# Performance work log

Hardware: AMD Instinct MI355X
Metric: run time of the kernel (lower is better)

## Reference

```python
import jax, jax.numpy as jnp
import numpy as np

GROUP_SIZE = 64  # quantization group size along in_features
RANK = 16
ALPHA = 1.0


def setup_inputs() -> dict:
    key = jax.random.key(0)
    ks = jax.random.split(key, 7)
    B, S, D_in, D_out = 4, 2048, 4096, 4096
    n_groups = D_in // GROUP_SIZE
    x = jax.random.normal(ks[0], (B, S, D_in), dtype=jnp.float32)
    qweight = jax.random.randint(ks[1], (D_out, D_in), 0, 16, dtype=jnp.int32)
    scales = jax.random.uniform(ks[2], (D_out, n_groups), dtype=jnp.float32) * 0.02
    zeros = jax.random.uniform(ks[3], (D_out, n_groups), dtype=jnp.float32) * 16.0
    lora_A = jax.random.normal(ks[4], (RANK, D_in), dtype=jnp.float32) / np.sqrt(D_in)
    lora_B = jax.random.normal(ks[5], (D_out, RANK), dtype=jnp.float32) * 0.01
    bias = jax.random.normal(ks[6], (D_out,), dtype=jnp.float32) * 0.02
    return {"x": x, "qweight": qweight, "scales": scales, "zeros": zeros,
            "lora_A": lora_A, "lora_B": lora_B, "bias": bias}


def _dequant(qweight, scales, zeros):
    # qweight: [O, I] int codes in [0,16); scales/zeros: [O, G] with G = I // GROUP_SIZE
    O, I = qweight.shape
    G = I // GROUP_SIZE
    q = qweight.astype(scales.dtype).reshape(O, G, GROUP_SIZE)
    w = (q - zeros[:, :, None]) * scales[:, :, None]
    return w.reshape(O, I)


def reference(x, qweight, scales, zeros, lora_A, lora_B, bias):
    # Base 4-bit dequantized matmul: y = x @ W^T
    W = _dequant(qweight, scales, zeros)            # [O, I]
    y = jnp.einsum('bsi,oi->bso', x, W)             # [B, S, O]
    # LoRA low-rank update: (alpha / rank) * (x @ A^T) @ B^T
    scaling = ALPHA / RANK
    lora = jnp.einsum('bsr,or->bso', jnp.einsum('bsi,ri->bsr', x, lora_A), lora_B)
    return y + scaling * lora + bias
```

## Files before the change

### kernel.cpp

```cpp
#include <hip/hip_runtime.h>
#include <stdint.h>
#include <stddef.h>

#define GM 8192
#define GN 4096
#define GK 4096
#define NGRP 64

typedef __bf16 bf16;
typedef __attribute__((ext_vector_type(8))) __bf16 bf16x8;
typedef __attribute__((ext_vector_type(4))) __bf16 bf16x4;
typedef __attribute__((ext_vector_type(4))) float floatx4;
typedef __attribute__((ext_vector_type(4))) int   intx4;
typedef __attribute__((ext_vector_type(8))) unsigned short ushortx8;
typedef __attribute__((ext_vector_type(4))) unsigned short ushortx4;

__device__ inline unsigned short f2bf(float f) {
  unsigned int u = __builtin_bit_cast(unsigned int, f);
  u += 0x7FFFu + ((u >> 16) & 1u);
  return (unsigned short)(u >> 16);
}
__device__ inline bf16x8 pack8(floatx4 a, floatx4 b) {
  ushortx8 u;
  u[0]=f2bf(a[0]); u[1]=f2bf(a[1]); u[2]=f2bf(a[2]); u[3]=f2bf(a[3]);
  u[4]=f2bf(b[0]); u[5]=f2bf(b[1]); u[6]=f2bf(b[2]); u[7]=f2bf(b[3]);
  return __builtin_bit_cast(bf16x8, u);
}
__device__ inline bf16x4 pack4(floatx4 a) {
  ushortx4 u;
  u[0]=f2bf(a[0]); u[1]=f2bf(a[1]); u[2]=f2bf(a[2]); u[3]=f2bf(a[3]);
  return __builtin_bit_cast(bf16x4, u);
}
__device__ inline void gll16(const void* g, void* l) {
  __builtin_amdgcn_global_load_lds(
      (const __attribute__((address_space(1))) void*)g,
      (__attribute__((address_space(3))) void*)l, 16, 0, 0);
}


__global__ __launch_bounds__(256) void qlora_prep_w(
    const int* __restrict__ qw, const float* __restrict__ scales,
    const float* __restrict__ zeros, const float* __restrict__ lA,
    const float* __restrict__ lB, bf16* __restrict__ wbf) {
  __shared__ __align__(16) float Al[16 * 256];
  __shared__ __align__(16) float Bl[32 * 16];
  const int tid = threadIdx.x;
  const int n0  = (blockIdx.x & 127) * 32;
  const int kc0 = (blockIdx.x >> 7) * 256;
  #pragma unroll
  for (int t = 0; t < 4; ++t) {
    int idx = tid + t * 256;
    int r = idx >> 6, c = idx & 63;
    *(floatx4*)&Al[r * 256 + c * 4] = *(const floatx4*)&lA[(size_t)r * GK + kc0 + c * 4];
  }
  if (tid < 128) {
    int r = tid >> 2, c = tid & 3;
    *(floatx4*)&Bl[r * 16 + c * 4] = *(const floatx4*)&lB[(size_t)(n0 + r) * 16 + c * 4];
  }
  __syncthreads();

  const int klane = tid & 63;
  const int wv    = tid >> 6;
  const int k  = klane * 4;
  const int kg = kc0 + k;
  const int kb = kg & ~63;
  const int g  = kg >> 6;

  floatx4 lacc[8] = {};
  #pragma unroll
  for (int r = 0; r < 16; ++r) {
    floatx4 av = *(const floatx4*)&Al[r * 256 + k];
    #pragma unroll
    for (int it = 0; it < 8; ++it)
      lacc[it] += av * Bl[(wv * 8 + it) * 16 + r];
  }

  #pragma unroll
  for (int it = 0; it < 8; ++it) {
    int n  = n0 + wv * 8 + it;
    intx4 qv = *(const intx4*)&qw[(size_t)n * GK + kg];
    float s = scales[n * NGRP + g];
    float z = zeros[n * NGRP + g];
    floatx4 w;
    w[0] = ((float)qv[0] - z) * s + 0.0625f * lacc[it][0];
    w[1] = ((float)qv[1] - z) * s + 0.0625f * lacc[it][1];
    w[2] = ((float)qv[2] - z) * s + 0.0625f * lacc[it][2];
    w[3] = ((float)qv[3] - z) * s + 0.0625f * lacc[it][3];
    int p = (((kg >> 3) & 7) ^ (n & 7)) << 3;
    *(bf16x4*)&wbf[(size_t)n * GK + kb + p + (kg & 7)] = pack4(w);
  }
}

__global__ __launch_bounds__(256) void qlora_prep_x(
    const float* __restrict__ x, bf16* __restrict__ xbf) {
  const int tid = threadIdx.x;
  const int xb  = blockIdx.x;
  #pragma unroll
  for (int t = 0; t < 4; ++t) {
    int fc = xb * 1024 + t * 256 + tid;
    int m  = fc >> 9;
    int rc = fc & 511;
    int p  = (rc & 7) ^ (m & 7);
    const float* src = x + ((size_t)fc << 3);
    floatx4 a = *(const floatx4*)src;
    floatx4 b = *(const floatx4*)(src + 4);
    *(bf16x8*)(xbf + (size_t)m * GK + ((rc >> 3) << 6) + (p << 3)) = pack8(a, b);
  }
}

__global__ __launch_bounds__(512, 1) void qlora_gemm_pre(
    const bf16* __restrict__ Abf, const bf16* __restrict__ Wbf,
    const float* __restrict__ bias, float* __restrict__ out) {
  __shared__ __align__(16) bf16 As[2][256 * 64];
  __shared__ __align__(16) bf16 Bs[2][256 * 64];
  const int tid  = threadIdx.x;
  const int wave = tid >> 6;
  const int lane = tid & 63;
  const int wr   = wave >> 2;
  const int wc   = wave & 3;

  const int flat = blockIdx.x;
  const int xcd  = flat & 7;
  const int j    = flat >> 3;
  const int m0   = (j >> 1) * 256;
  const int n0   = (xcd * 2 + (j & 1)) * 256;

  const int srow = tid >> 3;
  const int schk = tid & 7;
  const bf16* gA = Abf + (size_t)(m0 + srow) * GK + schk * 8;
  const bf16* gB = Wbf + (size_t)(n0 + srow) * GK + schk * 8;
  char* lA = (char*)&As[0][0] + srow * 128 + schk * 16;
  char* lB = (char*)&Bs[0][0] + srow * 128 + schk * 16;

  auto stageA = [&](int buf, int tk, int half) {
    #pragma unroll
    for (int r = 0; r < 2; ++r) {
      int rb = half * 128 + r * 64;
      gll16(gA + (size_t)rb * GK + tk * 64, lA + buf * 32768 + rb * 128);
    }
  };
  auto stageB = [&](int buf, int tk, int half) {
    #pragma unroll
    for (int r = 0; r < 2; ++r) {
      int rb = half * 128 + r * 64;
      gll16(gB + (size_t)rb * GK + tk * 64, lB + buf * 32768 + rb * 128);
    }
  };

  const int rs   = lane & 7;
  const int hi   = lane >> 4;
  const int rofs = (lane & 15) * 64;
  const int c0   = ((0 + hi) ^ rs) << 3;
  const int c1   = ((4 + hi) ^ rs) << 3;
  const int arow = wr * 64;
  const int brow = wc * 32;

  bf16x8 a0[4][2], a1[4][2], b0[2][2], b1[2][2];
  floatx4 acc[8][4] = {};

#define RD_A(DST, P, MH) { \
    const bf16* Ap_ = &As[P][(MH * 128 + arow) * 64 + rofs]; \
    _Pragma("unroll") \
    for (int mi = 0; mi < 4; ++mi) { \
      DST[mi][0] = *(const bf16x8*)(Ap_ + mi * 16 * 64 + c0); \
      DST[mi][1] = *(const bf16x8*)(Ap_ + mi * 16 * 64 + c1); \
    } }
#define RD_B(DST, P, NH) { \
    const bf16* Bp_ = &Bs[P][(NH * 128 + brow) * 64 + rofs]; \
    _Pragma("unroll") \
    for (int ni = 0; ni < 2; ++ni) { \
      DST[ni][0] = *(const bf16x8*)(Bp_ + ni * 16 * 64 + c0); \
      DST[ni][1] = *(const bf16x8*)(Bp_ + ni * 16 * 64 + c1); \
    } }
#define MFMA_PH(MH, NH, AR, BR) { \
    _Pragma("unroll") \
    for (int kk = 0; kk < 2; ++kk) \
      _Pragma("unroll") \
      for (int mi = 0; mi < 4; ++mi) \
        _Pragma("unroll") \
        for (int ni = 0; ni < 2; ++ni) \
          acc[MH * 4 + mi][NH * 2 + ni] = __builtin_amdgcn_mfma_f32_16x16x32_bf16( \
              AR[mi][kk], BR[ni][kk], acc[MH * 4 + mi][NH * 2 + ni], 0, 0, 0); \
  }
#define BAR() __builtin_amdgcn_s_barrier()
#define LGKM0() asm volatile("s_waitcnt lgkmcnt(0)" ::: "memory")
#define PRIO(N) __builtin_amdgcn_s_setprio(N)

  stageA(0, 0, 0); stageA(0, 0, 1); stageB(0, 0, 0); stageB(0, 0, 1);
  stageA(1, 1, 0); stageB(1, 1, 1); stageA(1, 1, 1);
  asm volatile("s_waitcnt vmcnt(6)" ::: "memory");
  BAR();

  for (int t = 0; t < 64; ++t) {
    const int p = t & 1;
    RD_A(a0, p, 0); RD_B(b0, p, 0);
    if (t < 63) stageB(1 - p, t + 1, 0);
    BAR(); LGKM0();
    PRIO(1); MFMA_PH(0, 0, a0, b0); PRIO(0);
    RD_B(b1, p, 1);
    BAR();
    if (t < 62) stageA(p, t + 2, 0);
    BAR(); LGKM0();
    PRIO(1); MFMA_PH(0, 1, a0, b1); PRIO(0);
    RD_A(a1, p, 1);
    BAR();
    if (t < 62) stageB(p, t + 2, 1);
    BAR(); LGKM0();
    PRIO(1); MFMA_PH(1, 1, a1, b1); PRIO(0);
    BAR();
    if (t < 62) {
      stageA(p, t + 2, 1);
      asm volatile("s_waitcnt vmcnt(6)" ::: "memory");
    } else {
      asm volatile("s_waitcnt vmcnt(0)" ::: "memory");
    }
    BAR();
    PRIO(1); MFMA_PH(1, 0, a1, b0); PRIO(0);
    BAR();
  }

#undef RD_A
#undef RD_B
#undef MFMA_PH
#undef BAR
#undef LGKM0
#undef PRIO

  const int quad = lane >> 4;
  const int col  = lane & 15;
  #pragma unroll
  for (int nh = 0; nh < 2; ++nh)
    #pragma unroll
    for (int ni = 0; ni < 2; ++ni) {
      const int gn = n0 + nh * 128 + wc * 32 + ni * 16 + col;
      const float bvv = bias[gn];
      #pragma unroll
      for (int mh = 0; mh < 2; ++mh)
        #pragma unroll
        for (int mi = 0; mi < 4; ++mi) {
          const int gm = m0 + mh * 128 + wr * 64 + mi * 16 + quad * 4;
          floatx4 a = acc[mh * 4 + mi][nh * 2 + ni];
          #pragma unroll
          for (int r = 0; r < 4; ++r)
            out[(size_t)(gm + r) * GN + gn] = a[r] + bvv;
        }
    }
}

__global__ void qlora_gemm_fb(const float* __restrict__ x, const int* __restrict__ qw,
                              const float* __restrict__ scales, const float* __restrict__ zeros,
                              const float* __restrict__ bias, float* __restrict__ out) {
  __shared__ __align__(16) bf16 As[128 * 64];
  __shared__ __align__(16) bf16 Bs[128 * 64];
  const int tid  = threadIdx.x;
  const int wave = tid >> 6;
  const int lane = tid & 63;
  const int m0 = blockIdx.x * 128;
  const int n0 = blockIdx.y * 128;
  const int wm = (wave >> 1) * 64;
  const int wn = (wave & 1) * 64;
  const int rsw = lane & 7;
  floatx4 acc[4][4] = {};
  for (int k0 = 0; k0 < GK; k0 += 64) {
    int row = tid >> 1, kh = (tid & 1) * 32;
    {
      const float* gx = x + (size_t)(m0 + row) * GK + k0 + kh;
      #pragma unroll
      for (int jj = 0; jj < 4; ++jj) {
        floatx4 a = *(const floatx4*)(gx + jj * 8);
        floatx4 b = *(const floatx4*)(gx + jj * 8 + 4);
        int p = (((kh >> 3) + jj) ^ (row & 7)) << 3;
        *(bf16x8*)&As[row * 64 + p] = pack8(a, b);
      }
    }
    {
      int n = n0 + row;
      int g = k0 >> 6;
      float s = scales[n * NGRP + g];
      float z = zeros[n * NGRP + g];
      const int* gq = qw + (size_t)n * GK + k0 + kh;
      #pragma unroll
      for (int jj = 0; jj < 4; ++jj) {
        intx4 q0 = *(const intx4*)(gq + jj * 8);
        intx4 q1 = *(const intx4*)(gq + jj * 8 + 4);
        floatx4 a, b;
        a[0]=((float)q0[0]-z)*s; a[1]=((float)q0[1]-z)*s; a[2]=((float)q0[2]-z)*s; a[3]=((float)q0[3]-z)*s;
        b[0]=((float)q1[0]-z)*s; b[1]=((float)q1[1]-z)*s; b[2]=((float)q1[2]-z)*s; b[3]=((float)q1[3]-z)*s;
        int p = (((kh >> 3) + jj) ^ (row & 7)) << 3;
        *(bf16x8*)&Bs[row * 64 + p] = pack8(a, b);
      }
    }
    __syncthreads();
    #pragma unroll
    for (int kk = 0; kk < 64; kk += 32) {
      const int cbase = kk >> 3;
      bf16x8 af[4], bfr[4];
      #pragma unroll
      for (int i = 0; i < 4; ++i)
        af[i] = *(const bf16x8*)&As[(wm + i * 16 + (lane & 15)) * 64
                                    + (((cbase + (lane >> 4)) ^ rsw) << 3)];
      #pragma unroll
      for (int i = 0; i < 4; ++i)
        bfr[i] = *(const bf16x8*)&Bs[(wn + i * 16 + (lane & 15)) * 64
                                     + (((cbase + (lane >> 4)) ^ rsw) << 3)];
      #pragma unroll
      for (int mi = 0; mi < 4; ++mi)
        #pragma unroll
        for (int ni = 0; ni < 4; ++ni)
          acc[mi][ni] = __builtin_amdgcn_mfma_f32_16x16x32_bf16(af[mi], bfr[ni], acc[mi][ni], 0, 0, 0);
    }
    __syncthreads();
  }
  const int quad = lane >> 4;
  const int col  = lane & 15;
  #pragma unroll
  for (int ni = 0; ni < 4; ++ni) {
    int gn = n0 + wn + ni * 16 + col;
    float bv = bias[gn];
    #pragma unroll
    for (int mi = 0; mi < 4; ++mi) {
      int gm = m0 + wm + mi * 16 + quad * 4;
      #pragma unroll
      for (int r = 0; r < 4; ++r)
        out[(size_t)(gm + r) * GN + gn] = acc[mi][ni][r] + bv;
    }
  }
}

extern "C" void kernel_launch(void* const* d_in, const int* in_sizes, int n_in,
                              void* d_out, int out_size, void* d_ws, size_t ws_size,
                              hipStream_t stream) {
  (void)in_sizes; (void)n_in; (void)out_size;
  const float* x      = (const float*)d_in[0];
  const int*   qw     = (const int*)d_in[1];
  const float* scales = (const float*)d_in[2];
  const float* zeros  = (const float*)d_in[3];
  const float* lA     = (const float*)d_in[4];
  const float* lB     = (const float*)d_in[5];
  const float* bias   = (const float*)d_in[6];
  float* out = (float*)d_out;

  const size_t xbf_bytes = (size_t)GM * GK * sizeof(bf16);
  const size_t wbf_bytes = (size_t)GN * GK * sizeof(bf16);
  char* ws = (char*)d_ws;

  if (ws_size >= xbf_bytes + wbf_bytes) {
    bf16* xbf = (bf16*)ws;
    bf16* wbf = (bf16*)(ws + xbf_bytes);
    qlora_prep_w<<<dim3(2048), 256, 0, stream>>>(qw, scales, zeros, lA, lB, wbf);
    qlora_prep_x<<<dim3(4096), 256, 0, stream>>>(x, xbf);
    qlora_gemm_pre<<<dim3((GM / 256) * (GN / 256)), 512, 0, stream>>>(xbf, wbf, bias, out);
  } else {
    qlora_gemm_fb<<<dim3(GM / 128, GN / 128), 256, 0, stream>>>(x, qw, scales, zeros, bias, out);
  }
}
```

Before: 499.1 us.

## Interleave LDS fragment reads with MFMA phases using sched_group_barrier

```diff
diff --git a/kernel.cpp b/kernel.cpp
--- a/kernel.cpp
+++ b/kernel.cpp
@@ -158,10 +158,10 @@
   bf16x8 a0[4][2], a1[4][2], b0[2][2], b1[2][2];
   floatx4 acc[8][4] = {};
 
-#define RD_A(DST, P, MH) { \
+#define RD_A_RANGE(DST, P, MH, M0, M1) { \
     const bf16* Ap_ = &As[P][(MH * 128 + arow) * 64 + rofs]; \
     _Pragma("unroll") \
-    for (int mi = 0; mi < 4; ++mi) { \
+    for (int mi = M0; mi < M1; ++mi) { \
       DST[mi][0] = *(const bf16x8*)(Ap_ + mi * 16 * 64 + c0); \
       DST[mi][1] = *(const bf16x8*)(Ap_ + mi * 16 * 64 + c1); \
     } }
@@ -184,28 +184,43 @@
   }
 #define BAR() __builtin_amdgcn_s_barrier()
 #define LGKM0() asm volatile("s_waitcnt lgkmcnt(0)" ::: "memory")
+#define SCHED0() __builtin_amdgcn_sched_barrier(0)
 #define PRIO(N) __builtin_amdgcn_s_setprio(N)
+#define SGB_U() { __builtin_amdgcn_sched_group_barrier(0x8, 2, 0); \
+                  __builtin_amdgcn_sched_group_barrier(0x100, 1, 0); }
+#define ILV6() { SGB_U(); SGB_U(); SGB_U(); SGB_U(); SGB_U(); SGB_U(); \
+                 __builtin_amdgcn_sched_group_barrier(0x8, 4, 0); }
+#define ILV8() { SGB_U(); SGB_U(); SGB_U(); SGB_U(); \
+                 SGB_U(); SGB_U(); SGB_U(); SGB_U(); }
 
   stageA(0, 0, 0); stageA(0, 0, 1); stageB(0, 0, 0); stageB(0, 0, 1);
   stageA(1, 1, 0); stageB(1, 1, 1); stageA(1, 1, 1);
   asm volatile("s_waitcnt vmcnt(6)" ::: "memory");
   BAR();
+  RD_A_RANGE(a0, 0, 0, 0, 4);
 
   for (int t = 0; t < 64; ++t) {
     const int p = t & 1;
-    RD_A(a0, p, 0); RD_B(b0, p, 0);
     if (t < 63) stageB(1 - p, t + 1, 0);
-    BAR(); LGKM0();
-    PRIO(1); MFMA_PH(0, 0, a0, b0); PRIO(0);
+    RD_B(b0, p, 0);
+    BAR(); LGKM0(); SCHED0();
+    PRIO(1);
+    MFMA_PH(0, 0, a0, b0);
     RD_B(b1, p, 1);
+    RD_A_RANGE(a1, p, 1, 0, 1);
+    PRIO(0);
+    ILV6();
     BAR();
     if (t < 62) stageA(p, t + 2, 0);
-    BAR(); LGKM0();
-    PRIO(1); MFMA_PH(0, 1, a0, b1); PRIO(0);
-    RD_A(a1, p, 1);
+    BAR(); LGKM0(); SCHED0();
+    PRIO(1);
+    MFMA_PH(0, 1, a0, b1);
+    RD_A_RANGE(a1, p, 1, 1, 4);
+    PRIO(0);
+    ILV6();
     BAR();
     if (t < 62) stageB(p, t + 2, 1);
-    BAR(); LGKM0();
+    BAR(); LGKM0(); SCHED0();
     PRIO(1); MFMA_PH(1, 1, a1, b1); PRIO(0);
     BAR();
     if (t < 62) {
@@ -214,17 +229,25 @@
     } else {
       asm volatile("s_waitcnt vmcnt(0)" ::: "memory");
     }
+    BAR(); SCHED0();
+    PRIO(1);
+    MFMA_PH(1, 0, a1, b0);
+    RD_A_RANGE(a0, 1 - p, 0, 0, 4);
+    PRIO(0);
+    ILV8();
     BAR();
-    PRIO(1); MFMA_PH(1, 0, a1, b0); PRIO(0);
-    BAR();
-  }
-
-#undef RD_A
+  }
+
+#undef RD_A_RANGE
 #undef RD_B
 #undef MFMA_PH
 #undef BAR
 #undef LGKM0
+#undef SCHED0
 #undef PRIO
+#undef SGB_U
+#undef ILV6
+#undef ILV8
 
   const int quad = lane >> 4;
   const int col  = lane & 15;
```

Result: slower. 572.1 us (+14.6%).
